# Kernel tuning notes

Measured on AMD Instinct MI355X. Metric: run time of the kernel, lower is better.

## Reference

```python
import jax, jax.numpy as jnp
import numpy as np

B, T, F = 16384, 48, 4
UNITS = 256
OUT_STEPS = 24


def setup_inputs() -> dict:
    key = jax.random.key(0)
    ks = jax.random.split(key, 6)
    s_x = 1.0 / np.sqrt(F)
    s_h = 1.0 / np.sqrt(UNITS)
    return {
        "x": jax.random.normal(ks[0], (B, T, F), jnp.float32),
        "Wx": jax.random.normal(ks[1], (F, 4 * UNITS), jnp.float32) * s_x,
        "Wh": jax.random.normal(ks[2], (UNITS, 4 * UNITS), jnp.float32) * s_h,
        "b": jnp.zeros((4 * UNITS,), jnp.float32),
        "Wd": jax.random.normal(ks[3], (UNITS, F), jnp.float32) * s_h,
        "bd": jnp.zeros((F,), jnp.float32),
    }


def _lstm_cell(xt, h, c, Wx, Wh, b):
    # Keras LSTMCell gate order: i, f, g(cell candidate), o
    z = xt @ Wx + h @ Wh + b  # [B, 4*units]
    i, f, g, o = jnp.split(z, 4, axis=-1)
    i = jax.nn.sigmoid(i)
    f = jax.nn.sigmoid(f)
    g = jnp.tanh(g)
    o = jax.nn.sigmoid(o)
    c_new = f * c + i * g
    h_new = o * jnp.tanh(c_new)
    return h_new, c_new


def reference(x, Wx, Wh, b, Wd, bd):
    bsz = x.shape[0]
    h0 = jnp.zeros((bsz, UNITS), x.dtype)
    c0 = jnp.zeros((bsz, UNITS), x.dtype)

    # --- warmup: run LSTM over the input window, keep final state ---
    def warm_step(carry, xt):
        h, c = carry
        h, c = _lstm_cell(xt, h, c, Wx, Wh, b)
        return (h, c), None

    (h, c), _ = jax.lax.scan(warm_step, (h0, c0), jnp.swapaxes(x, 0, 1))
    pred0 = h @ Wd + bd  # first prediction [B, F]

    def ar_step(carry, _):
        h, c, pred = carry
        h, c = _lstm_cell(pred, h, c, Wx, Wh, b)
        pred = h @ Wd + bd
        return (h, c, pred), pred

    _, preds = jax.lax.scan(ar_step, (h, c, pred0), None, length=OUT_STEPS - 1)
    preds = jnp.concatenate([pred0[None], preds], axis=0)  # [out_steps, B, F]
    return jnp.swapaxes(preds, 0, 1)  # [B, out_steps, F]
```

## Files before the change

### kernel.cpp

```cpp
#include <hip/hip_runtime.h>


typedef unsigned short u16;
typedef __attribute__((ext_vector_type(8))) short bf16x8;
typedef __attribute__((ext_vector_type(16))) float f32x16;

#define PITCH 296
#define HB 18944
#define WARM 48
#define STEPS 71
#define LOG2E  1.442695041f
#define LOG2E2 2.885390082f

__device__ __forceinline__ u16 f2bf(float f) {
    unsigned u = __float_as_uint(f);
    u += 0x7FFFu + ((u >> 16) & 1u);
    return (u16)(u >> 16);
}

__device__ __forceinline__ void sync_lds() {
    asm volatile("s_waitcnt lgkmcnt(0)\n\ts_barrier" ::: "memory");
}

__global__ void prep_weights(const float* __restrict__ Wx,
                             const float* __restrict__ Wh,
                             const float* __restrict__ b,
                             const float* __restrict__ Wd,
                             const float* __restrict__ bd,
                             u16* __restrict__ whext,
                             u16* __restrict__ wdp) {
    int idx = blockIdx.x * 256 + threadIdx.x;
    if (idx < 36864) {
        int lane = idx & 63;
        int frag = idx >> 6;
        int wv = frag & 7;
        int g = (frag >> 3) & 3;
        int kt = frag >> 5;
        int k0 = kt * 16 + (lane >> 5) * 8;
        int n = 256 * g + 32 * wv + (lane & 31);
        float sc = (g == 2) ? LOG2E2 : LOG2E;
        u16 v[8];
#pragma unroll
        for (int j = 0; j < 8; ++j) {
            int k = k0 + j;
            float f = 0.0f;
            if (k < 256) f = Wh[k * 1024 + n];
            else if (k < 260) f = Wx[(k - 256) * 1024 + n];
            else if (k == 260) f = b[n];
            v[j] = f2bf(f * sc);
        }
        ushort4* dst = (ushort4*)(whext + (size_t)idx * 8);
        dst[0] = make_ushort4(v[0], v[1], v[2], v[3]);
        dst[1] = make_ushort4(v[4], v[5], v[6], v[7]);
    } else if (idx < 36864 + 1152) {
        int id2 = idx - 36864;
        int lane = id2 & 63;
        int kt = id2 >> 6;
        int k0 = kt * 16 + (lane >> 5) * 8;
        int f_ = lane & 31;
        u16 v[8];
#pragma unroll
        for (int j = 0; j < 8; ++j) {
            int k = k0 + j;
            float f = 0.0f;
            if (f_ < 4) {
                if (k < 256) f = Wd[k * 4 + f_];
                else if (k == 260) f = bd[f_];
            }
            v[j] = f2bf(f);
        }
        ushort4* dst = (ushort4*)(wdp + (size_t)id2 * 8);
        dst[0] = make_ushort4(v[0], v[1], v[2], v[3]);
        dst[1] = make_ushort4(v[4], v[5], v[6], v[7]);
    }
}

#define WLOAD(DST, KTV) do {                                                  \
    const char* _wpk = wp + (size_t)(KTV) * 32768;                            \
    _Pragma("unroll") for (int g = 0; g < 4; ++g)                             \
        DST[g] = *(const bf16x8*)(_wpk + voff[g]);                            \
} while (0)

#define HLOAD(DST, KTV) do {                                                  \
    DST[0] = *(const bf16x8*)&hr[hrow0 + (KTV) * 16];                         \
    DST[1] = *(const bf16x8*)&hr[hrow1 + (KTV) * 16];                         \
} while (0)

#define MT(WA, HBX)                                                           \
    _Pragma("unroll") for (int m = 0; m < 2; ++m)                             \
    _Pragma("unroll") for (int g = 0; g < 4; ++g)                             \
        acc[m][g] = __builtin_amdgcn_mfma_f32_32x32x16_bf16(                  \
            WA[g], HBX[m], acc[m][g], 0, 0, 0);

__global__ __launch_bounds__(512, 2) void lstm_main(
    const float* __restrict__ x, const u16* __restrict__ whext,
    const u16* __restrict__ wdp, float* __restrict__ out) {
    __shared__ __align__(16) u16 hbuf[2 * HB];

    const int tid = threadIdx.x;
    const int w = tid >> 6;
    const int l = tid & 63;
    const int l31 = l & 31;
    const int lh = l >> 5;
    const long long rowBase = (long long)blockIdx.x * 64;

    {
        int4 z = make_int4(0, 0, 0, 0);
        for (int i = tid; i < 4736; i += 512) ((int4*)hbuf)[i] = z;
    }
    sync_lds();
    if (tid < 64) {
        hbuf[tid * PITCH + 260] = (u16)0x3F80;
        hbuf[HB + tid * PITCH + 260] = (u16)0x3F80;
        const float4 xv = *(const float4*)(x + (rowBase + tid) * 192);
        u16* p = &hbuf[tid * PITCH + 256];
        p[0] = f2bf(xv.x); p[1] = f2bf(xv.y); p[2] = f2bf(xv.z); p[3] = f2bf(xv.w);
    }

    const char* __restrict__ wp = (const char*)whext;
    const char* __restrict__ dp = (const char*)wdp;
    int voff[4];
#pragma unroll
    for (int g = 0; g < 4; ++g) voff[g] = ((g * 8 + w) * 64 + l) * 16;
    const int hrow0 = l31 * PITCH + lh * 8;
    const int hrow1 = (32 + l31) * PITCH + lh * 8;

    f32x16 c[2] = {};
    bf16x8 awA[4], awB[4], awC[4];
    WLOAD(awA, 0);
    WLOAD(awB, 1);

    for (int step = 0; step < STEPS; ++step) {
        const u16* hr = hbuf + (step & 1) * HB;
        u16* hw = hbuf + ((step & 1) ^ 1) * HB;
        sync_lds();

        f32x16 acc[2][4] = {};
        bf16x8 hbA[2], hbB[2], hbC[2];
        HLOAD(hbA, 0);
        HLOAD(hbB, 1);

#pragma unroll 1
        for (int t = 0; t < 15; t += 3) {
            WLOAD(awC, t + 2); HLOAD(hbC, t + 2);
            MT(awA, hbA);
            WLOAD(awA, t + 3); HLOAD(hbA, t + 3);
            MT(awB, hbB);
            WLOAD(awB, t + 4); HLOAD(hbB, t + 4);
            MT(awC, hbC);
        }
        WLOAD(awC, 17); HLOAD(hbC, 17);
        MT(awA, hbA);
        WLOAD(awA, 0);
        MT(awB, hbB);
        WLOAD(awB, 1);
        MT(awC, hbC);

#pragma unroll
        for (int m = 0; m < 2; ++m) {
            const int hwrow = (32 * m + l31) * PITCH + 32 * w + 4 * lh;
#pragma unroll
            for (int q = 0; q < 4; ++q) {
                u16 hh[4];
#pragma unroll
                for (int rr = 0; rr < 4; ++rr) {
                    const int r = q * 4 + rr;
                    float ei = __builtin_amdgcn_exp2f(-acc[m][0][r]);
                    float ef = __builtin_amdgcn_exp2f(-acc[m][1][r]);
                    float eg = __builtin_amdgcn_exp2f(-acc[m][2][r]);
                    float eo = __builtin_amdgcn_exp2f(-acc[m][3][r]);
                    float fv  = __builtin_amdgcn_rcpf(1.0f + ef);
                    float rig = __builtin_amdgcn_rcpf((1.0f + ei) * (1.0f + eg));
                    float cn  = c[m][r] * fv + (1.0f - eg) * rig;
                    c[m][r] = cn;
                    float ec = __builtin_amdgcn_exp2f(-LOG2E2 * cn);
                    float roc = __builtin_amdgcn_rcpf((1.0f + eo) * (1.0f + ec));
                    hh[rr] = f2bf((1.0f - ec) * roc);
                }
                *(ushort4*)&hw[hwrow + 8 * q] = make_ushort4(hh[0], hh[1], hh[2], hh[3]);
            }
        }

        if (step < WARM - 1) {
            if (w == 0) {
                const float4 xv = *(const float4*)(x + (rowBase + l) * 192 + (step + 1) * 4);
                u16* p = &hw[l * PITCH + 256];
                p[0] = f2bf(xv.x); p[1] = f2bf(xv.y); p[2] = f2bf(xv.z); p[3] = f2bf(xv.w);
            }
        } else {
            sync_lds();
            if (w < 2) {
                f32x16 pacc = {};
                const int prow = (32 * w + l31) * PITCH + lh * 8;
#pragma unroll
                for (int kt = 0; kt < 18; ++kt) {
                    bf16x8 hbp = *(const bf16x8*)&hw[prow + kt * 16];
                    bf16x8 wap = *(const bf16x8*)(dp + ((size_t)kt * 64 + l) * 16);
                    pacc = __builtin_amdgcn_mfma_f32_32x32x16_bf16(wap, hbp, pacc, 0, 0, 0);
                }
                if (lh == 0) {
                    int s = step - (WARM - 1);
                    int batch = 32 * w + l31;
                    *(float4*)&out[((rowBase + batch) * 24 + s) * 4] =
                        make_float4(pacc[0], pacc[1], pacc[2], pacc[3]);
                    *(ushort4*)&hw[batch * PITCH + 256] =
                        make_ushort4(f2bf(pacc[0]), f2bf(pacc[1]), f2bf(pacc[2]), f2bf(pacc[3]));
                }
            }
        }
    }
}

extern "C" void kernel_launch(void* const* d_in, const int* in_sizes, int n_in,
                              void* d_out, int out_size, void* d_ws, size_t ws_size,
                              hipStream_t stream) {
    const float* x  = (const float*)d_in[0];
    const float* Wx = (const float*)d_in[1];
    const float* Wh = (const float*)d_in[2];
    const float* b  = (const float*)d_in[3];
    const float* Wd = (const float*)d_in[4];
    const float* bd = (const float*)d_in[5];
    float* out = (float*)d_out;

    u16* whext = (u16*)d_ws;
    u16* wdp = (u16*)((char*)d_ws + 589824);

    prep_weights<<<(36864 + 1152 + 255) / 256, 256, 0, stream>>>(Wx, Wh, b, Wd, bd, whext, wdp);
    lstm_main<<<256, 512, 0, stream>>>(x, whext, wdp, out);
}
```

Measured before the change: 826.2 us.

## Replace per-step block barriers with LDS flag-based producer/consumer sync and staggered k-tiles

Removes the per-step workgroup barriers and replaces them with per-wave LDS flags: each wave posts when its h slice or its x/prediction columns are written. Consumers spin-wait only on the specific k-tile they need next. Each wave starts its K loop at a different tile (2*w) so it can consume tiles already published by its neighbours, letting waves drift instead of lockstepping. The K loop drops from 18 to 17 tiles, and the unused zero tile 17 is removed from both matmuls. The spin-waits with s_sleep and the workgroup-scope atomics add polling overhead and memory-ordering risk, including possible overwrite hazards on the double-buffered h.

```diff
diff --git a/kernel.cpp b/kernel.cpp
--- a/kernel.cpp
+++ b/kernel.cpp
@@ -20,6 +20,15 @@
 
 __device__ __forceinline__ void sync_lds() {
     asm volatile("s_waitcnt lgkmcnt(0)\n\ts_barrier" ::: "memory");
+}
+
+__device__ __forceinline__ void wait_ge(int* f, int target) {
+    while (__hip_atomic_load(f, __ATOMIC_ACQUIRE, __HIP_MEMORY_SCOPE_WORKGROUP) < target)
+        __builtin_amdgcn_s_sleep(1);
+}
+__device__ __forceinline__ void post(int* f, int v, int lane) {
+    if (lane == 0)
+        __hip_atomic_store(f, v, __ATOMIC_RELEASE, __HIP_MEMORY_SCOPE_WORKGROUP);
 }
 
 __global__ void prep_weights(const float* __restrict__ Wx,
@@ -75,15 +84,15 @@
     }
 }
 
-#define WLOAD(DST, KTV) do {                                                  \
-    const char* _wpk = wp + (size_t)(KTV) * 32768;                            \
+#define WLOADT(DST, T) do {                                                   \
+    const char* _wk = wp + ((size_t)(T) << 15);                               \
     _Pragma("unroll") for (int g = 0; g < 4; ++g)                             \
-        DST[g] = *(const bf16x8*)(_wpk + voff[g]);                            \
+        DST[g] = *(const bf16x8*)(_wk + voff[g]);                             \
 } while (0)
 
-#define HLOAD(DST, KTV) do {                                                  \
-    DST[0] = *(const bf16x8*)&hr[hrow0 + (KTV) * 16];                         \
-    DST[1] = *(const bf16x8*)&hr[hrow1 + (KTV) * 16];                         \
+#define HLOADT(DST, T) do {                                                   \
+    DST[0] = *(const bf16x8*)&hr[hrow0 + (T) * 16];                           \
+    DST[1] = *(const bf16x8*)&hr[hrow1 + (T) * 16];                           \
 } while (0)
 
 #define MT(WA, HBX)                                                           \
@@ -92,10 +101,19 @@
         acc[m][g] = __builtin_amdgcn_mfma_f32_32x32x16_bf16(                  \
             WA[g], HBX[m], acc[m][g], 0, 0, 0);
 
+#define GUARD(I) do {                                                         \
+    if ((I) < 16) wait_ge(&Ff[((2 * w + (I)) & 15) >> 1], step);              \
+    else { wait_ge(&Xf[0], step); wait_ge(&Xf[1], step); }                    \
+} while (0)
+
 __global__ __launch_bounds__(512, 2) void lstm_main(
     const float* __restrict__ x, const u16* __restrict__ whext,
     const u16* __restrict__ wdp, float* __restrict__ out) {
-    __shared__ __align__(16) u16 hbuf[2 * HB];
+    __shared__ __align__(16) unsigned char smem[75904];
+    u16* hbuf = (u16*)smem;
+    int* Ff = (int*)(smem + 75776);
+    int* Pf = Ff + 8;
+    int* Xf = Ff + 16;
 
     const int tid = threadIdx.x;
     const int w = tid >> 6;
@@ -106,7 +124,7 @@
 
     {
         int4 z = make_int4(0, 0, 0, 0);
-        for (int i = tid; i < 4736; i += 512) ((int4*)hbuf)[i] = z;
+        for (int i = tid; i < 4744; i += 512) ((int4*)smem)[i] = z;
     }
     sync_lds();
     if (tid < 64) {
@@ -116,6 +134,7 @@
         u16* p = &hbuf[tid * PITCH + 256];
         p[0] = f2bf(xv.x); p[1] = f2bf(xv.y); p[2] = f2bf(xv.z); p[3] = f2bf(xv.w);
     }
+    sync_lds();
 
     const char* __restrict__ wp = (const char*)whext;
     const char* __restrict__ dp = (const char*)wdp;
@@ -124,37 +143,40 @@
     for (int g = 0; g < 4; ++g) voff[g] = ((g * 8 + w) * 64 + l) * 16;
     const int hrow0 = l31 * PITCH + lh * 8;
     const int hrow1 = (32 + l31) * PITCH + lh * 8;
+    const int t0 = 2 * w, t1 = 2 * w + 1;
 
     f32x16 c[2] = {};
     bf16x8 awA[4], awB[4], awC[4];
-    WLOAD(awA, 0);
-    WLOAD(awB, 1);
+    WLOADT(awA, t0);
+    WLOADT(awB, t1);
 
     for (int step = 0; step < STEPS; ++step) {
         const u16* hr = hbuf + (step & 1) * HB;
         u16* hw = hbuf + ((step & 1) ^ 1) * HB;
-        sync_lds();
 
         f32x16 acc[2][4] = {};
         bf16x8 hbA[2], hbB[2], hbC[2];
-        HLOAD(hbA, 0);
-        HLOAD(hbB, 1);
+        HLOADT(hbA, t0);
+        HLOADT(hbB, t1);
 
 #pragma unroll 1
-        for (int t = 0; t < 15; t += 3) {
-            WLOAD(awC, t + 2); HLOAD(hbC, t + 2);
+        for (int i = 0; i < 15; i += 3) {
+            GUARD(i + 2); { int t = (2 * w + i + 2) & 15; WLOADT(awC, t); HLOADT(hbC, t); }
             MT(awA, hbA);
-            WLOAD(awA, t + 3); HLOAD(hbA, t + 3);
+            GUARD(i + 3); { int t = (2 * w + i + 3) & 15; WLOADT(awA, t); HLOADT(hbA, t); }
             MT(awB, hbB);
-            WLOAD(awB, t + 4); HLOAD(hbB, t + 4);
+            { int i4 = i + 4; GUARD(i4); int t = (i4 < 16) ? ((2 * w + i4) & 15) : 16;
+              WLOADT(awB, t); HLOADT(hbB, t); }
             MT(awC, hbC);
         }
-        WLOAD(awC, 17); HLOAD(hbC, 17);
+        post(Pf + w, step + 1, l);
         MT(awA, hbA);
-        WLOAD(awA, 0);
+        WLOADT(awA, t0);
         MT(awB, hbB);
-        WLOAD(awB, 1);
-        MT(awC, hbC);
+        WLOADT(awB, t1);
+
+#pragma unroll 1
+        for (int c2 = 0; c2 < 8; ++c2) wait_ge(Pf + c2, step);
 
 #pragma unroll
         for (int m = 0; m < 2; ++m) {
@@ -180,20 +202,24 @@
                 *(ushort4*)&hw[hwrow + 8 * q] = make_ushort4(hh[0], hh[1], hh[2], hh[3]);
             }
         }
+        post(Ff + w, step + 1, l);
 
         if (step < WARM - 1) {
             if (w == 0) {
                 const float4 xv = *(const float4*)(x + (rowBase + l) * 192 + (step + 1) * 4);
                 u16* p = &hw[l * PITCH + 256];
                 p[0] = f2bf(xv.x); p[1] = f2bf(xv.y); p[2] = f2bf(xv.z); p[3] = f2bf(xv.w);
+                post(Xf + 0, step + 1, l);
+                post(Xf + 1, step + 1, l);
             }
         } else {
-            sync_lds();
             if (w < 2) {
+#pragma unroll 1
+                for (int p2 = 0; p2 < 8; ++p2) wait_ge(Ff + p2, step + 1);
                 f32x16 pacc = {};
                 const int prow = (32 * w + l31) * PITCH + lh * 8;
 #pragma unroll
-                for (int kt = 0; kt < 18; ++kt) {
+                for (int kt = 0; kt < 17; ++kt) {
                     bf16x8 hbp = *(const bf16x8*)&hw[prow + kt * 16];
                     bf16x8 wap = *(const bf16x8*)(dp + ((size_t)kt * 64 + l) * 16);
                     pacc = __builtin_amdgcn_mfma_f32_32x32x16_bf16(wap, hbp, pacc, 0, 0, 0);
@@ -206,6 +232,7 @@
                     *(ushort4*)&hw[batch * PITCH + 256] =
                         make_ushort4(f2bf(pacc[0]), f2bf(pacc[1]), f2bf(pacc[2]), f2bf(pacc[3]));
                 }
+                post(Xf + w, step + 1, l);
             }
         }
     }
```

Result: slower. 887.1 us (+7.4%).

## Skip zero-padded k-tile, merge gate reciprocals, use packed bf16 conversion

Applied to the files above, without the earlier changes.

The recurrent matmul and dense projection now iterate 17 k-tiles instead of 18, because the last tile held only zero padding beyond the bias row. The register pipeline drops from three to two stages. The gate math merges the forget and input reciprocals into one rcp. Packed v_cvt_pk_bf16_f32 replaces manual rounding, and the next x slice is prefetched before the barrier. Shallower prefetch may expose more load latency, while fewer registers may help scheduling.

```diff
diff --git a/kernel.cpp b/kernel.cpp
--- a/kernel.cpp
+++ b/kernel.cpp
@@ -16,6 +16,12 @@
     unsigned u = __float_as_uint(f);
     u += 0x7FFFu + ((u >> 16) & 1u);
     return (u16)(u >> 16);
+}
+
+__device__ __forceinline__ unsigned pk_bf16(float a, float b) {
+    unsigned d;
+    asm("v_cvt_pk_bf16_f32 %0, %1, %2" : "=v"(d) : "v"(a), "v"(b));
+    return d;
 }
 
 __device__ __forceinline__ void sync_lds() {
@@ -75,15 +81,15 @@
     }
 }
 
-#define WLOAD(DST, KTV) do {                                                  \
-    const char* _wpk = wp + (size_t)(KTV) * 32768;                            \
+#define WLOADT(DST, T) do {                                                   \
+    const char* _wk = wp + ((size_t)(T) << 15);                               \
     _Pragma("unroll") for (int g = 0; g < 4; ++g)                             \
-        DST[g] = *(const bf16x8*)(_wpk + voff[g]);                            \
+        DST[g] = *(const bf16x8*)(_wk + voff[g]);                             \
 } while (0)
 
-#define HLOAD(DST, KTV) do {                                                  \
-    DST[0] = *(const bf16x8*)&hr[hrow0 + (KTV) * 16];                         \
-    DST[1] = *(const bf16x8*)&hr[hrow1 + (KTV) * 16];                         \
+#define HLOADT(DST, T) do {                                                   \
+    DST[0] = *(const bf16x8*)&hr[hrow0 + (T) * 16];                           \
+    DST[1] = *(const bf16x8*)&hr[hrow1 + (T) * 16];                           \
 } while (0)
 
 #define MT(WA, HBX)                                                           \
@@ -113,8 +119,8 @@
         hbuf[tid * PITCH + 260] = (u16)0x3F80;
         hbuf[HB + tid * PITCH + 260] = (u16)0x3F80;
         const float4 xv = *(const float4*)(x + (rowBase + tid) * 192);
-        u16* p = &hbuf[tid * PITCH + 256];
-        p[0] = f2bf(xv.x); p[1] = f2bf(xv.y); p[2] = f2bf(xv.z); p[3] = f2bf(xv.w);
+        uint2* p = (uint2*)&hbuf[tid * PITCH + 256];
+        *p = make_uint2(pk_bf16(xv.x, xv.y), pk_bf16(xv.z, xv.w));
     }
 
     const char* __restrict__ wp = (const char*)whext;
@@ -126,66 +132,75 @@
     const int hrow1 = (32 + l31) * PITCH + lh * 8;
 
     f32x16 c[2] = {};
-    bf16x8 awA[4], awB[4], awC[4];
-    WLOAD(awA, 0);
-    WLOAD(awB, 1);
+    bf16x8 awA[4], awB[4];
+    WLOADT(awA, 0);
+    WLOADT(awB, 1);
 
     for (int step = 0; step < STEPS; ++step) {
         const u16* hr = hbuf + (step & 1) * HB;
         u16* hw = hbuf + ((step & 1) ^ 1) * HB;
+
+        float4 xv = make_float4(0.f, 0.f, 0.f, 0.f);
+        if (w == 0 && step < WARM - 1)
+            xv = *(const float4*)(x + (rowBase + l) * 192 + (step + 1) * 4);
+
         sync_lds();
 
         f32x16 acc[2][4] = {};
-        bf16x8 hbA[2], hbB[2], hbC[2];
-        HLOAD(hbA, 0);
-        HLOAD(hbB, 1);
+        bf16x8 hbA[2], hbB[2];
+        HLOADT(hbA, 0);
+        HLOADT(hbB, 1);
 
 #pragma unroll 1
-        for (int t = 0; t < 15; t += 3) {
-            WLOAD(awC, t + 2); HLOAD(hbC, t + 2);
+        for (int t = 0; t < 13; t += 2) {
             MT(awA, hbA);
-            WLOAD(awA, t + 3); HLOAD(hbA, t + 3);
+            WLOADT(awA, t + 2); HLOADT(hbA, t + 2);
             MT(awB, hbB);
-            WLOAD(awB, t + 4); HLOAD(hbB, t + 4);
-            MT(awC, hbC);
-        }
-        WLOAD(awC, 17); HLOAD(hbC, 17);
+            WLOADT(awB, t + 3); HLOADT(hbB, t + 3);
+        }
         MT(awA, hbA);
-        WLOAD(awA, 0);
+        WLOADT(awA, 16); HLOADT(hbA, 16);
         MT(awB, hbB);
-        WLOAD(awB, 1);
-        MT(awC, hbC);
+        WLOADT(awB, 1);
+        MT(awA, hbA);
+        WLOADT(awA, 0);
 
 #pragma unroll
         for (int m = 0; m < 2; ++m) {
             const int hwrow = (32 * m + l31) * PITCH + 32 * w + 4 * lh;
 #pragma unroll
             for (int q = 0; q < 4; ++q) {
-                u16 hh[4];
-#pragma unroll
-                for (int rr = 0; rr < 4; ++rr) {
-                    const int r = q * 4 + rr;
-                    float ei = __builtin_amdgcn_exp2f(-acc[m][0][r]);
-                    float ef = __builtin_amdgcn_exp2f(-acc[m][1][r]);
-                    float eg = __builtin_amdgcn_exp2f(-acc[m][2][r]);
-                    float eo = __builtin_amdgcn_exp2f(-acc[m][3][r]);
-                    float fv  = __builtin_amdgcn_rcpf(1.0f + ef);
-                    float rig = __builtin_amdgcn_rcpf((1.0f + ei) * (1.0f + eg));
-                    float cn  = c[m][r] * fv + (1.0f - eg) * rig;
-                    c[m][r] = cn;
-                    float ec = __builtin_amdgcn_exp2f(-LOG2E2 * cn);
-                    float roc = __builtin_amdgcn_rcpf((1.0f + eo) * (1.0f + ec));
-                    hh[rr] = f2bf((1.0f - ec) * roc);
+                unsigned pk[2];
+#pragma unroll
+                for (int hp = 0; hp < 2; ++hp) {
+                    float h2[2];
+#pragma unroll
+                    for (int rr = 0; rr < 2; ++rr) {
+                        const int r = q * 4 + hp * 2 + rr;
+                        float ei = __builtin_amdgcn_exp2f(-acc[m][0][r]);
+                        float ef = __builtin_amdgcn_exp2f(-acc[m][1][r]);
+                        float eg = __builtin_amdgcn_exp2f(-acc[m][2][r]);
+                        float eo = __builtin_amdgcn_exp2f(-acc[m][3][r]);
+                        float ai = 1.0f + ei, af = 1.0f + ef;
+                        float ag = 1.0f + eg, ao = 1.0f + eo;
+                        float P  = ai * ag;
+                        float rD = __builtin_amdgcn_rcpf(P * af);
+                        float cn = fmaf(c[m][r] * P, rD, (1.0f - eg) * af * rD);
+                        c[m][r] = cn;
+                        float ec = __builtin_amdgcn_exp2f(-LOG2E2 * cn);
+                        float rE = __builtin_amdgcn_rcpf(ao * (1.0f + ec));
+                        h2[rr] = (1.0f - ec) * rE;
+                    }
+                    pk[hp] = pk_bf16(h2[0], h2[1]);
                 }
-                *(ushort4*)&hw[hwrow + 8 * q] = make_ushort4(hh[0], hh[1], hh[2], hh[3]);
+                *(uint2*)&hw[hwrow + 8 * q] = make_uint2(pk[0], pk[1]);
             }
         }
 
         if (step < WARM - 1) {
             if (w == 0) {
-                const float4 xv = *(const float4*)(x + (rowBase + l) * 192 + (step + 1) * 4);
-                u16* p = &hw[l * PITCH + 256];
-                p[0] = f2bf(xv.x); p[1] = f2bf(xv.y); p[2] = f2bf(xv.z); p[3] = f2bf(xv.w);
+                uint2* p = (uint2*)&hw[l * PITCH + 256];
+                *p = make_uint2(pk_bf16(xv.x, xv.y), pk_bf16(xv.z, xv.w));
             }
         } else {
             sync_lds();
@@ -193,7 +208,7 @@
                 f32x16 pacc = {};
                 const int prow = (32 * w + l31) * PITCH + lh * 8;
 #pragma unroll
-                for (int kt = 0; kt < 18; ++kt) {
+                for (int kt = 0; kt < 17; ++kt) {
                     bf16x8 hbp = *(const bf16x8*)&hw[prow + kt * 16];
                     bf16x8 wap = *(const bf16x8*)(dp + ((size_t)kt * 64 + l) * 16);
                     pacc = __builtin_amdgcn_mfma_f32_32x32x16_bf16(wap, hbp, pacc, 0, 0, 0);
@@ -203,8 +218,8 @@
                     int batch = 32 * w + l31;
                     *(float4*)&out[((rowBase + batch) * 24 + s) * 4] =
                         make_float4(pacc[0], pacc[1], pacc[2], pacc[3]);
-                    *(ushort4*)&hw[batch * PITCH + 256] =
-                        make_ushort4(f2bf(pacc[0]), f2bf(pacc[1]), f2bf(pacc[2]), f2bf(pacc[3]));
+                    *(uint2*)&hw[batch * PITCH + 256] =
+                        make_uint2(pk_bf16(pacc[0], pacc[1]), pk_bf16(pacc[2], pacc[3]));
                 }
             }
         }
```

New measurement: 751.1 us. 9.1% less time.
